# Kernel optimization log

Measured on AMD Instinct MI355X. Metric: run time of the kernel, lower is better.

The kernel has to match this reference:

```python
import jax, jax.numpy as jnp
import numpy as np

B, S, D = 2, 2048, 1024
H, DK = 16, 64


def setup_inputs() -> dict:
    key = jax.random.key(0)
    ks = jax.random.split(key, 10)
    scale = D ** -0.5
    x = jax.random.normal(ks[0], (B, S, D), dtype=jnp.float32)
    mask = jax.random.randint(ks[1], (B, S), 0, 2) > 0  # True = masked positions
    Wq = jax.random.normal(ks[2], (D, H * DK), dtype=jnp.float32) * scale
    Wk = jax.random.normal(ks[3], (D, H * DK), dtype=jnp.float32) * scale
    Wv = jax.random.normal(ks[4], (D, H * DK), dtype=jnp.float32) * scale
    Wo = jax.random.normal(ks[5], (H * DK, D), dtype=jnp.float32) * scale
    bq = jnp.zeros((H * DK,), jnp.float32)
    bk = jnp.zeros((H * DK,), jnp.float32)
    bv = jnp.zeros((H * DK,), jnp.float32)
    bo = jnp.zeros((D,), jnp.float32)
    return {"x": x, "mask": mask, "Wq": Wq, "bq": bq, "Wk": Wk, "bk": bk,
            "Wv": Wv, "bv": bv, "Wo": Wo, "bo": bo}


def reference(x, mask, Wq, bq, Wk, bk, Wv, bv, Wo, bo):
    b, s, _ = x.shape
    # Linear + activation (dropout is identity at eval)
    q = jax.nn.relu(x @ Wq + bq).reshape(b, s, H, DK)
    k = jax.nn.relu(x @ Wk + bk).reshape(b, s, H, DK)
    v = jax.nn.relu(x @ Wv + bv).reshape(b, s, H, DK)
    # scores: [B, H, Sq, Sk]
    attn = jnp.einsum("bqhd,bkhd->bhqk", q, k) * (DK ** -0.5)
    # NOTE: original uses masked_fill(mask, 1e-9) BEFORE softmax (not -inf)
    attn = jnp.where(mask[:, None, None, :], jnp.float32(1e-9), attn)
    attn = jax.nn.softmax(attn, axis=-1)
    out = jnp.einsum("bhqk,bkhd->bqhd", attn, v).reshape(b, s, H * DK)
    return jax.nn.relu(out @ Wo + bo)
```

## Files before the change

kernel.cpp:

```cpp
#include <hip/hip_runtime.h>
#include <stdint.h>

typedef __attribute__((ext_vector_type(8))) short short8;
typedef __attribute__((ext_vector_type(4))) short short4b;
typedef __attribute__((ext_vector_type(4))) float f32x4;

#define MFMA16(a, b, c) __builtin_amdgcn_mfma_f32_16x16x32_bf16((a), (b), (c), 0, 0, 0)

#if defined(__HIP_DEVICE_COMPILE__)
  #if __has_builtin(__builtin_amdgcn_mfma_f32_16x16x16bf16_1k)
    #define MFMA16K16(a, b, c) __builtin_amdgcn_mfma_f32_16x16x16bf16_1k((a), (b), (c), 0, 0, 0)
  #else
    #define MFMA16K16(a, b, c) __builtin_amdgcn_mfma_f32_16x16x16_bf16((a), (b), (c), 0, 0, 0)
  #endif
  #if __has_builtin(__builtin_amdgcn_exp2f)
    #define EXP2(x) __builtin_amdgcn_exp2f(x)
  #else
    #define EXP2(x) exp2f(x)
  #endif
#else
  #define MFMA16K16(a, b, c) (c)
  #define EXP2(x) exp2f(x)
#endif

#define SCL_F (0.125f * 1.44269504f)

__device__ __forceinline__ float b2f(unsigned short u) {
    union { unsigned u; float f; } c; c.u = ((unsigned)u) << 16; return c.f;
}
__device__ __forceinline__ unsigned short f2b(float f) {
    union { float f; unsigned u; } c; c.f = f;
    unsigned r = c.u + 0x7FFF + ((c.u >> 16) & 1);
    return (unsigned short)(r >> 16);
}
__device__ __forceinline__ unsigned f_as_u(float f) {
    union { float f; unsigned u; } c; c.f = f; return c.u;
}

__device__ __forceinline__ void g2lds16(const unsigned short* g, unsigned lds_byte_off) {
    __builtin_amdgcn_global_load_lds(
        (const __attribute__((address_space(1))) void*)(uintptr_t)g,
        (__attribute__((address_space(3))) void*)(uintptr_t)lds_byte_off,
        16, 0, 0);
}

__global__ void detect_dtype(const unsigned short* __restrict__ x, int* __restrict__ flag) {
    __shared__ int cnt;
    if (threadIdx.x == 0) cnt = 0;
    __syncthreads();
    int insane = 0;
    #pragma unroll
    for (int j = 0; j < 4; ++j) {
        unsigned short u = x[threadIdx.x * 4 + j];
        int e = (u >> 7) & 0xFF;
        if ((e >= 1 && e <= 90) || e >= 165) insane++;
    }
    atomicAdd(&cnt, insane);
    __syncthreads();
    if (threadIdx.x == 0) *flag = (cnt > 128) ? 1 : 0;
}

__global__ __launch_bounds__(256) void convtrans_k(const void* __restrict__ s0, const void* __restrict__ s1,
                                                   const void* __restrict__ s2, const void* __restrict__ s3,
                                                   const void* __restrict__ b0, const void* __restrict__ b1,
                                                   const void* __restrict__ b2, const void* __restrict__ b3s,
                                                   const void* __restrict__ xsrc,
                                                   unsigned short* __restrict__ xdst,
                                                   unsigned short* __restrict__ dstBase,
                                                   unsigned short* __restrict__ dstB3,
                                                   unsigned short* __restrict__ dstBo,
                                                   const int* __restrict__ flag) {
    const int z = blockIdx.z;
    if (z >= 5) {
        if (!*flag) return;
        const int slice = z - 5;
        const size_t i0 = (size_t)slice * 524288 + (blockIdx.y * 16 + blockIdx.x) * 2048 + threadIdx.x * 8;
        const float* s = (const float*)xsrc;
        float4 f0 = *(const float4*)&s[i0];
        float4 f1 = *(const float4*)&s[i0 + 4];
        union { short8 v; unsigned short u[8]; } o;
        o.u[0] = f2b(f0.x); o.u[1] = f2b(f0.y); o.u[2] = f2b(f0.z); o.u[3] = f2b(f0.w);
        o.u[4] = f2b(f1.x); o.u[5] = f2b(f1.y); o.u[6] = f2b(f1.z); o.u[7] = f2b(f1.w);
        *(short8*)&xdst[i0] = o.v;
        return;
    }
    if (z == 4) {
        if (blockIdx.y != 0 || blockIdx.x >= 4) return;
        const int w = blockIdx.x;
        const void* src = (w == 0) ? b0 : (w == 1) ? b1 : (w == 2) ? b2 : b3s;
        const float bscl = (w == 0) ? SCL_F : 1.0f;
        #pragma unroll
        for (int j = 0; j < 4; ++j) {
            const int i = threadIdx.x * 4 + j;
            float fv = (*flag) ? ((const float*)src)[i] : b2f(((const unsigned short*)src)[i]);
            unsigned short v = f2b(fv * bscl);
            if (w < 3) dstB3[w * 1024 + i] = v;
            else dstBo[i] = v;
        }
        return;
    }
    __shared__ __align__(16) unsigned short tile[64 * 72];
    const void* src = (z == 0) ? s0 : (z == 1) ? s1 : (z == 2) ? s2 : s3;
    unsigned short* dst = dstBase + (size_t)z * 1024 * 1024;
    const float wscl = (z == 0) ? SCL_F : 1.0f;
    const int tid = threadIdx.x;
    const int r0 = blockIdx.y * 64, c0 = blockIdx.x * 64;
    const int rb = tid >> 3, c = (tid & 7) * 8;
    if (*flag) {
        const float* s = (const float*)src;
        #pragma unroll
        for (int it = 0; it < 2; ++it) {
            int rr = it * 32 + rb;
            float4 f0 = *(const float4*)&s[(size_t)(r0 + rr) * 1024 + c0 + c];
            float4 f1 = *(const float4*)&s[(size_t)(r0 + rr) * 1024 + c0 + c + 4];
            unsigned short* t = &tile[rr * 72 + c];
            t[0] = f2b(f0.x * wscl); t[1] = f2b(f0.y * wscl); t[2] = f2b(f0.z * wscl); t[3] = f2b(f0.w * wscl);
            t[4] = f2b(f1.x * wscl); t[5] = f2b(f1.y * wscl); t[6] = f2b(f1.z * wscl); t[7] = f2b(f1.w * wscl);
        }
    } else if (z == 0) {
        const unsigned short* s = (const unsigned short*)src;
        #pragma unroll
        for (int it = 0; it < 2; ++it) {
            int rr = it * 32 + rb;
            union { short8 v; unsigned short u[8]; } in;
            in.v = *(const short8*)&s[(size_t)(r0 + rr) * 1024 + c0 + c];
            unsigned short* t = &tile[rr * 72 + c];
            #pragma unroll
            for (int j = 0; j < 8; ++j) t[j] = f2b(b2f(in.u[j]) * SCL_F);
        }
    } else {
        const unsigned short* s = (const unsigned short*)src;
        #pragma unroll
        for (int it = 0; it < 2; ++it) {
            int rr = it * 32 + rb;
            *(short8*)&tile[rr * 72 + c] = *(const short8*)&s[(size_t)(r0 + rr) * 1024 + c0 + c];
        }
    }
    __syncthreads();
    #pragma unroll
    for (int it = 0; it < 2; ++it) {
        int n = it * 32 + rb, k8 = c;
        union { short8 s; unsigned short u[8]; } tmp;
        #pragma unroll
        for (int j = 0; j < 8; ++j) tmp.u[j] = tile[(k8 + j) * 72 + n];
        *(short8*)&dst[(size_t)(c0 + n) * 1024 + r0 + k8] = tmp.s;
    }
}

__global__ __launch_bounds__(256) void gemm_qkv(const unsigned short* __restrict__ A,
                                                const void* __restrict__ Araw,
                                                const unsigned short* __restrict__ BT,
                                                const unsigned short* __restrict__ bias,
                                                unsigned short* __restrict__ qkv,
                                                unsigned short* __restrict__ VtG,
                                                const int* __restrict__ mask,
                                                const int* __restrict__ flag,
                                                int K) {
    __shared__ __align__(16) unsigned short smem[24576];
    const int tid = threadIdx.x;
    const int wave = tid >> 6, lane = tid & 63;
    const int quad = lane >> 4, l16 = lane & 15;
    const int wm = wave >> 1, wn = wave & 1;
    const int m0 = blockIdx.y * 128, n0 = blockIdx.x * 128;

    const unsigned short* Ause = (Araw != nullptr && *flag == 0) ? (const unsigned short*)Araw : A;

    f32x4 acc[4][4];
    #pragma unroll
    for (int i = 0; i < 4; i++)
        #pragma unroll
        for (int j = 0; j < 4; j++) acc[i][j] = (f32x4){0.f, 0.f, 0.f, 0.f};

    const int r2 = lane >> 3, sl = lane & 7;
    const int sp = sl ^ r2;
    const int rowl = r2 * 2 + (sp >> 2);
    const int col8 = (sp & 3) * 8;
    const unsigned short* gA0 = Ause + (size_t)(m0 + wave * 32 + rowl) * K + col8;
    const unsigned short* gA1 = gA0 + (size_t)16 * K;
    const unsigned short* gB0 = BT + (size_t)(n0 + wave * 32 + rowl) * K + col8;
    const unsigned short* gB1 = gB0 + (size_t)16 * K;

    const unsigned sA = (unsigned)(uintptr_t)&smem[0];
    const unsigned sB = sA + 24576;
    unsigned lA0 = sA + wave * 2048;
    unsigned lA1 = sA + 8192 + wave * 2048;
    unsigned lA2 = sA + 16384 + wave * 2048;
    unsigned lB0 = sB + wave * 2048;
    unsigned lB1 = sB + 8192 + wave * 2048;
    unsigned lB2 = sB + 16384 + wave * 2048;
    const unsigned short* pA0 = &smem[0];
    const unsigned short* pA1 = &smem[4096];
    const unsigned short* pA2 = &smem[8192];
    const unsigned short* pB0 = &smem[12288];
    const unsigned short* pB1 = &smem[16384];
    const unsigned short* pB2 = &smem[20480];

    const int swz = (((l16 & 1) << 2) | quad) ^ (l16 >> 1);
    const int hp  = l16 >> 1;

    g2lds16(gA0, lA0); g2lds16(gA1, lA0 + 1024);
    g2lds16(gB0, lB0); g2lds16(gB1, lB0 + 1024);
    if (32 < K) {
        g2lds16(gA0 + 32, lA1); g2lds16(gA1 + 32, lA1 + 1024);
        g2lds16(gB0 + 32, lB1); g2lds16(gB1 + 32, lB1 + 1024);
    }
    if (64 < K) {
        g2lds16(gA0 + 64, lA2); g2lds16(gA1 + 64, lA2 + 1024);
        g2lds16(gB0 + 64, lB2); g2lds16(gB1 + 64, lB2 + 1024);
    }

    for (int k0 = 0; k0 < K; k0 += 32) {
        if (k0 + 64 < K)       asm volatile("s_waitcnt vmcnt(8)" ::: "memory");
        else if (k0 + 32 < K)  asm volatile("s_waitcnt vmcnt(4)" ::: "memory");
        else                   asm volatile("s_waitcnt vmcnt(0)" ::: "memory");
        __builtin_amdgcn_s_barrier();

        short8 af[4], bf[4];
        #pragma unroll
        for (int i = 0; i < 4; i++) af[i] = *(const short8*)&pA0[(wm * 32 + i * 8 + hp) * 64 + swz * 8];
        #pragma unroll
        for (int j = 0; j < 4; j++) bf[j] = *(const short8*)&pB0[(wn * 32 + j * 8 + hp) * 64 + swz * 8];
        #pragma unroll
        for (int i = 0; i < 4; i++)
            #pragma unroll
            for (int j = 0; j < 4; j++)
                acc[i][j] = MFMA16(af[i], bf[j], acc[i][j]);

        __builtin_amdgcn_s_barrier();

        if (k0 + 96 < K) {
            g2lds16(gA0 + k0 + 96, lA0); g2lds16(gA1 + k0 + 96, lA0 + 1024);
            g2lds16(gB0 + k0 + 96, lB0); g2lds16(gB1 + k0 + 96, lB0 + 1024);
        }
        unsigned tu;
        tu = lA0; lA0 = lA1; lA1 = lA2; lA2 = tu;
        tu = lB0; lB0 = lB1; lB1 = lB2; lB2 = tu;
        const unsigned short* tp;
        tp = pA0; pA0 = pA1; pA1 = pA2; pA2 = tp;
        tp = pB0; pB0 = pB1; pB1 = pB2; pB2 = tp;
    }

    unsigned short* epi = &smem[0];
    if (n0 >= 2048) {
        #pragma unroll
        for (int j = 0; j < 4; j++) {
            const int cl = wn * 64 + j * 16 + l16;
            const float bj = b2f(bias[n0 + cl]);
            #pragma unroll
            for (int i = 0; i < 4; i++) {
                const int rl = wm * 64 + i * 16 + quad * 4;
                #pragma unroll
                for (int r = 0; r < 4; r++) {
                    float v = acc[i][j][r] + bj;
                    v = v > 0.f ? v : 0.f;
                    epi[cl * 132 + rl + r] = f2b(v);
                }
            }
        }
        __syncthreads();
        const int cl = tid >> 1, half = (tid & 1) * 64;
        const int colg = n0 + cl;
        const int h  = (colg - 2048) >> 6;
        const int dk = (colg - 2048) & 63;
        const int bb = m0 >> 11;
        unsigned short* dst = &VtG[((size_t)(bb * 16 + h) * 64 + dk) * 2048 + (m0 & 2047) + half];
        const unsigned short* src = &epi[cl * 132 + half];
        #pragma unroll
        for (int k = 0; k < 8; k++) *(short8*)&dst[k * 8] = *(const short8*)&src[k * 8];
    } else {
        #pragma unroll
        for (int j = 0; j < 4; j++) {
            const int cl = wn * 64 + j * 16 + l16;
            const float bj = b2f(bias[n0 + cl]);
            #pragma unroll
            for (int i = 0; i < 4; i++) {
                const int rl = wm * 64 + i * 16 + quad * 4;
                #pragma unroll
                for (int r = 0; r < 4; r++) {
                    float v = acc[i][j][r] + bj;
                    v = v > 0.f ? v : 0.f;
                    epi[(rl + r) * 132 + cl] = f2b(v);
                }
            }
        }
        __syncthreads();
        const int row = tid >> 1, half = (tid & 1) * 64;
        const int rowg = m0 + row;
        const int mz = (n0 >= 1024) && mask[rowg];
        unsigned short* dst = &qkv[(size_t)rowg * 3072 + n0 + half];
        const unsigned short* src = &epi[row * 132 + half];
        const short8 zero = {0, 0, 0, 0, 0, 0, 0, 0};
        #pragma unroll
        for (int k = 0; k < 8; k++) *(short8*)&dst[k * 8] = mz ? zero : *(const short8*)&src[k * 8];
    }
}

__global__ __launch_bounds__(256) void gemm64_bias_relu(const unsigned short* __restrict__ A,
                                                        const unsigned short* __restrict__ BT,
                                                        const unsigned short* __restrict__ bias,
                                                        void* __restrict__ C,
                                                        const int* __restrict__ flag,
                                                        int N, int K) {
    __shared__ __align__(16) unsigned short As[3][64 * 32];
    __shared__ __align__(16) unsigned short Bs[3][128 * 32];
    const int tid = threadIdx.x;
    const int wave = tid >> 6, lane = tid & 63;
    const int quad = lane >> 4, l16 = lane & 15;
    const int wm = wave >> 1, wn = wave & 1;
    const int m0 = blockIdx.y * 64, n0 = blockIdx.x * 128;

    f32x4 acc[2][4];
    #pragma unroll
    for (int i = 0; i < 2; i++)
        #pragma unroll
        for (int j = 0; j < 4; j++) acc[i][j] = (f32x4){0.f, 0.f, 0.f, 0.f};

    const int r2 = lane >> 3, sl = lane & 7;
    const int sp = sl ^ r2;
    const int rowl = r2 * 2 + (sp >> 2);
    const int col8 = (sp & 3) * 8;
    const unsigned short* gA0 = A + (size_t)(m0 + wave * 16 + rowl) * K + col8;
    const unsigned short* gB0 = BT + (size_t)(n0 + wave * 32 + rowl) * K + col8;
    const unsigned short* gB1 = gB0 + (size_t)16 * K;

    unsigned lA0 = (unsigned)(uintptr_t)&As[0][0] + wave * 1024;
    unsigned lA1 = (unsigned)(uintptr_t)&As[1][0] + wave * 1024;
    unsigned lA2 = (unsigned)(uintptr_t)&As[2][0] + wave * 1024;
    unsigned lB0 = (unsigned)(uintptr_t)&Bs[0][0] + wave * 2048;
    unsigned lB1 = (unsigned)(uintptr_t)&Bs[1][0] + wave * 2048;
    unsigned lB2 = (unsigned)(uintptr_t)&Bs[2][0] + wave * 2048;
    const unsigned short* pA0 = &As[0][0];
    const unsigned short* pA1 = &As[1][0];
    const unsigned short* pA2 = &As[2][0];
    const unsigned short* pB0 = &Bs[0][0];
    const unsigned short* pB1 = &Bs[1][0];
    const unsigned short* pB2 = &Bs[2][0];

    const int swz = (((l16 & 1) << 2) | quad) ^ (l16 >> 1);
    const int hp  = l16 >> 1;

    g2lds16(gA0, lA0);
    g2lds16(gB0, lB0); g2lds16(gB1, lB0 + 1024);
    if (32 < K) {
        g2lds16(gA0 + 32, lA1);
        g2lds16(gB0 + 32, lB1); g2lds16(gB1 + 32, lB1 + 1024);
    }
    if (64 < K) {
        g2lds16(gA0 + 64, lA2);
        g2lds16(gB0 + 64, lB2); g2lds16(gB1 + 64, lB2 + 1024);
    }

    for (int k0 = 0; k0 < K; k0 += 32) {
        if (k0 + 64 < K)       asm volatile("s_waitcnt vmcnt(6)" ::: "memory");
        else if (k0 + 32 < K)  asm volatile("s_waitcnt vmcnt(3)" ::: "memory");
        else                   asm volatile("s_waitcnt vmcnt(0)" ::: "memory");
        __builtin_amdgcn_s_barrier();

        short8 af[2], bf[4];
        #pragma unroll
        for (int i = 0; i < 2; i++) af[i] = *(const short8*)&pA0[(wm * 16 + i * 8 + hp) * 64 + swz * 8];
        #pragma unroll
        for (int j = 0; j < 4; j++) bf[j] = *(const short8*)&pB0[(wn * 32 + j * 8 + hp) * 64 + swz * 8];
        #pragma unroll
        for (int i = 0; i < 2; i++)
            #pragma unroll
            for (int j = 0; j < 4; j++)
                acc[i][j] = MFMA16(af[i], bf[j], acc[i][j]);

        __builtin_amdgcn_s_barrier();

        if (k0 + 96 < K) {
            g2lds16(gA0 + k0 + 96, lA0);
            g2lds16(gB0 + k0 + 96, lB0); g2lds16(gB1 + k0 + 96, lB0 + 1024);
        }
        unsigned tu;
        tu = lA0; lA0 = lA1; lA1 = lA2; lA2 = tu;
        tu = lB0; lB0 = lB1; lB1 = lB2; lB2 = tu;
        const unsigned short* tp;
        tp = pA0; pA0 = pA1; pA1 = pA2; pA2 = tp;
        tp = pB0; pB0 = pB1; pB1 = pB2; pB2 = tp;
    }

    const int f32out = (*flag != 0);
    #pragma unroll
    for (int j = 0; j < 4; j++) {
        const int col = n0 + wn * 64 + j * 16 + l16;
        const float bj = b2f(bias[col]);
        #pragma unroll
        for (int i = 0; i < 2; i++) {
            const int rowb = m0 + wm * 32 + i * 16 + quad * 4;
            #pragma unroll
            for (int r = 0; r < 4; r++) {
                float v = acc[i][j][r] + bj;
                v = v > 0.f ? v : 0.f;
                if (f32out) ((float*)C)[(size_t)(rowb + r) * N + col] = v;
                else ((unsigned short*)C)[(size_t)(rowb + r) * N + col] = f2b(v);
            }
        }
    }
}

#define ATTN_TILE(Kbuf, Vbuf)                                                            \
    do {                                                                                 \
        __builtin_amdgcn_s_setprio(1);                                                   \
        f32x4 sA[4], sB[4];                                                              \
        _Pragma("unroll")                                                                \
        for (int t = 0; t < 4; ++t) {                                                    \
            const short8 kb0 = *(const short8*)&(Kbuf)[(((t * 16 + l16) * 64) + quad * 8) ^ rx];       \
            const short8 kb1 = *(const short8*)&(Kbuf)[(((t * 16 + l16) * 64) + 32 + quad * 8) ^ rx];  \
            f32x4 z = (f32x4){0.f, 0.f, 0.f, 0.f};                                       \
            sA[t] = MFMA16(kb1, qa1, MFMA16(kb0, qa0, z));                               \
            sB[t] = MFMA16(kb1, qb1, MFMA16(kb0, qb0, z));                               \
        }                                                                                \
        short4b vb[4][4];                                                                \
        _Pragma("unroll")                                                                \
        for (int t = 0; t < 4; ++t)                                                      \
            _Pragma("unroll")                                                            \
            for (int n = 0; n < 4; ++n)                                                  \
                vb[t][n] = *(const short4b*)&(Vbuf)[(((n * 16 + l16) * 64) + t * 16 + quad * 4) ^ rx]; \
        _Pragma("unroll")                                                                \
        for (int t = 0; t < 4; ++t) {                                                    \
            float pA[4], pB[4];                                                          \
            _Pragma("unroll")                                                            \
            for (int r = 0; r < 4; ++r) {                                                \
                pA[r] = EXP2(sA[t][r]);                                                  \
                pB[r] = EXP2(sB[t][r]);                                                  \
            }                                                                            \
            union { unsigned u[2]; short4b s; } fa, fb;                                  \
            fa.u[0] = __builtin_amdgcn_perm(f_as_u(pA[1]), f_as_u(pA[0]), 0x07060302u);  \
            fa.u[1] = __builtin_amdgcn_perm(f_as_u(pA[3]), f_as_u(pA[2]), 0x07060302u);  \
            fb.u[0] = __builtin_amdgcn_perm(f_as_u(pB[1]), f_as_u(pB[0]), 0x07060302u);  \
            fb.u[1] = __builtin_amdgcn_perm(f_as_u(pB[3]), f_as_u(pB[2]), 0x07060302u);  \
            _Pragma("unroll")                                                            \
            for (int n = 0; n < 4; ++n) {                                                \
                oA[n] = MFMA16K16(fa.s, vb[t][n], oA[n]);                                \
                oB[n] = MFMA16K16(fb.s, vb[t][n], oB[n]);                                \
            }                                                                            \
            sumA = MFMA16K16(fa.s, ones, sumA);                                          \
            sumB = MFMA16K16(fb.s, ones, sumB);                                          \
        }                                                                                \
        __builtin_amdgcn_s_setprio(0);                                                   \
    } while (0)

__global__ __launch_bounds__(256) void attn_kernel(const unsigned short* __restrict__ qkv,
                                                   const unsigned short* __restrict__ VtG,
                                                   unsigned short* __restrict__ out) {
    __shared__ __align__(16) unsigned short Ks[2][64 * 64];
    __shared__ __align__(16) unsigned short Vs[2][64 * 64];

    const int l = blockIdx.y * 16 + blockIdx.x;
    const int v = (l & 7) * 64 + (l >> 3);
    const int qt = v & 15, bh = v >> 4;
    const int b = bh >> 4, h = bh & 15;
    const int tid = threadIdx.x, wave = tid >> 6, lane = tid & 63;
    const int quad = lane >> 4, l16 = lane & 15;

    const int qrowA = qt * 128 + wave * 16 + l16;
    const unsigned short* qpA = qkv + (size_t)(b * 2048 + qrowA) * 3072 + h * 64;
    const unsigned short* qpB = qpA + (size_t)64 * 3072;
    const short8 qa0 = *(const short8*)(qpA + quad * 8);
    const short8 qa1 = *(const short8*)(qpA + 32 + quad * 8);
    const short8 qb0 = *(const short8*)(qpB + quad * 8);
    const short8 qb1 = *(const short8*)(qpB + 32 + quad * 8);

    f32x4 oA[4], oB[4], sumA, sumB;
    #pragma unroll
    for (int n = 0; n < 4; n++) { oA[n] = (f32x4){0.f,0.f,0.f,0.f}; oB[n] = (f32x4){0.f,0.f,0.f,0.f}; }
    sumA = (f32x4){0.f,0.f,0.f,0.f};
    sumB = (f32x4){0.f,0.f,0.f,0.f};

    const short4b ones = { (short)0x3F80, (short)0x3F80, (short)0x3F80, (short)0x3F80 };

    const int srow = tid >> 2;
    const int scol = (tid & 3) * 16;
    const int sxor = (srow & 7) << 3;
    const unsigned short* kg = qkv + (size_t)(b * 2048 + srow) * 3072 + 1024 + h * 64 + scol;
    const unsigned short* vg = VtG + (size_t)(bh * 64 + srow) * 2048 + scol;
    const size_t kstep = (size_t)64 * 3072;
    const int sidx0 = (srow * 64 + scol) ^ sxor;
    const int sidx1 = (srow * 64 + scol + 8) ^ sxor;
    unsigned short* wK0a = &Ks[0][sidx0];  unsigned short* wK1a = &Ks[0][sidx1];
    unsigned short* wV0a = &Vs[0][sidx0];  unsigned short* wV1a = &Vs[0][sidx1];
    unsigned short* wK0b = &Ks[1][sidx0];  unsigned short* wK1b = &Ks[1][sidx1];
    unsigned short* wV0b = &Vs[1][sidx0];  unsigned short* wV1b = &Vs[1][sidx1];

    const int rx = (l16 & 7) << 3;

    short8 rkA0 = *(const short8*)(kg);
    short8 rkA1 = *(const short8*)(kg + 8);
    short8 rvA0 = *(const short8*)(vg);
    short8 rvA1 = *(const short8*)(vg + 8);
    *(short8*)wK0a = rkA0;  *(short8*)wK1a = rkA1;
    *(short8*)wV0a = rvA0;  *(short8*)wV1a = rvA1;
    short8 rkB0 = *(const short8*)(kg + kstep);
    short8 rkB1 = *(const short8*)(kg + kstep + 8);
    short8 rvB0 = *(const short8*)(vg + 64);
    short8 rvB1 = *(const short8*)(vg + 64 + 8);
    __syncthreads();

    for (int kt = 0; kt < 32; kt += 2) {
        *(short8*)wK0b = rkB0;  *(short8*)wK1b = rkB1;
        *(short8*)wV0b = rvB0;  *(short8*)wV1b = rvB1;
        if (kt + 2 < 32) {
            rkA0 = *(const short8*)(kg + (kt + 2) * kstep);
            rkA1 = *(const short8*)(kg + (kt + 2) * kstep + 8);
            rvA0 = *(const short8*)(vg + (kt + 2) * 64);
            rvA1 = *(const short8*)(vg + (kt + 2) * 64 + 8);
        }
        ATTN_TILE(Ks[0], Vs[0]);
        __syncthreads();

        if (kt + 2 < 32) {
            *(short8*)wK0a = rkA0;  *(short8*)wK1a = rkA1;
            *(short8*)wV0a = rvA0;  *(short8*)wV1a = rvA1;
        }
        if (kt + 3 < 32) {
            rkB0 = *(const short8*)(kg + (kt + 3) * kstep);
            rkB1 = *(const short8*)(kg + (kt + 3) * kstep + 8);
            rvB0 = *(const short8*)(vg + (kt + 3) * 64);
            rvB1 = *(const short8*)(vg + (kt + 3) * 64 + 8);
        }
        ATTN_TILE(Ks[1], Vs[1]);
        __syncthreads();
    }

    float invA[4], invB[4];
    #pragma unroll
    for (int r = 0; r < 4; ++r) { invA[r] = 1.0f / sumA[r]; invB[r] = 1.0f / sumB[r]; }
    #pragma unroll
    for (int n = 0; n < 4; n++)
        #pragma unroll
        for (int r = 0; r < 4; r++) {
            const int row = qt * 128 + wave * 16 + quad * 4 + r;
            out[(size_t)(b * 2048 + row) * 1024 + h * 64 + n * 16 + l16] = f2b(oA[n][r] * invA[r]);
            out[(size_t)(b * 2048 + row + 64) * 1024 + h * 64 + n * 16 + l16] = f2b(oB[n][r] * invB[r]);
        }
}

extern "C" void kernel_launch(void* const* d_in, const int* in_sizes, int n_in,
                              void* d_out, int out_size, void* d_ws, size_t ws_size,
                              hipStream_t stream) {
    const void* x  = d_in[0];
    const int*  mk = (const int*)d_in[1];
    const void* Wq = d_in[2]; const void* bq = d_in[3];
    const void* Wk = d_in[4]; const void* bk = d_in[5];
    const void* Wv = d_in[6]; const void* bv = d_in[7];
    const void* Wo = d_in[8]; const void* bo = d_in[9];

    char* wsb = (char*)d_ws;
    int* flag = (int*)wsb;
    unsigned short* W0 = (unsigned short*)(wsb + 64);

    const size_t M1 = 1024u * 1024u;
    const size_t M4 = 4096u * 1024u;
    unsigned short* xb  = W0;
    unsigned short* WT  = xb + M4;
    unsigned short* WoT = WT + 3 * M1;
    unsigned short* b3  = WoT + M1;
    unsigned short* bob = b3 + 4096;
    unsigned short* qkv = bob + 1024;
    unsigned short* VtG = qkv + (size_t)4096 * 3072;
    unsigned short* abf = xb;

    detect_dtype<<<1, 256, 0, stream>>>((const unsigned short*)x, flag);

    convtrans_k<<<dim3(16, 16, 13), 256, 0, stream>>>(Wq, Wk, Wv, Wo, bq, bk, bv, bo,
                                                      x, xb, WT, b3, bob, flag);

    gemm_qkv<<<dim3(24, 32), 256, 0, stream>>>(xb, x, WT, b3, qkv, VtG, mk, flag, 1024);
    attn_kernel<<<dim3(16, 32), 256, 0, stream>>>(qkv, VtG, abf);
    gemm64_bias_relu<<<dim3(8, 64), 256, 0, stream>>>(abf, WoT, bob, d_out, flag, 1024, 1024);
}
```

Baseline: 196.2 us.

## Switch output GEMM to double-buffered BK=64 tiles without LDS swizzle

The gemm64_bias_relu kernel moves from a triple-buffered K=32 pipeline to a double-buffered K=64 pipeline, with two MFMA sub-steps per barrier pair. This halves the number of barriers and wait points per K and issues larger batches of global-to-LDS loads. It also drops the XOR swizzle in favour of a plain row-major LDS layout with 128-byte row stride. That layout risks LDS bank conflicts on the short8 fragment reads, and the shallower prefetch depth gives less latency hiding.

```diff
diff --git a/kernel.cpp b/kernel.cpp
--- a/kernel.cpp
+++ b/kernel.cpp
@@ -301,8 +301,8 @@
                                                         void* __restrict__ C,
                                                         const int* __restrict__ flag,
                                                         int N, int K) {
-    __shared__ __align__(16) unsigned short As[3][64 * 32];
-    __shared__ __align__(16) unsigned short Bs[3][128 * 32];
+    __shared__ __align__(16) unsigned short As[2][64 * 64];
+    __shared__ __align__(16) unsigned short Bs[2][128 * 64];
     const int tid = threadIdx.x;
     const int wave = tid >> 6, lane = tid & 63;
     const int quad = lane >> 4, l16 = lane & 15;
@@ -315,70 +315,66 @@
         #pragma unroll
         for (int j = 0; j < 4; j++) acc[i][j] = (f32x4){0.f, 0.f, 0.f, 0.f};
 
-    const int r2 = lane >> 3, sl = lane & 7;
-    const int sp = sl ^ r2;
-    const int rowl = r2 * 2 + (sp >> 2);
-    const int col8 = (sp & 3) * 8;
-    const unsigned short* gA0 = A + (size_t)(m0 + wave * 16 + rowl) * K + col8;
-    const unsigned short* gB0 = BT + (size_t)(n0 + wave * 32 + rowl) * K + col8;
-    const unsigned short* gB1 = gB0 + (size_t)16 * K;
-
-    unsigned lA0 = (unsigned)(uintptr_t)&As[0][0] + wave * 1024;
-    unsigned lA1 = (unsigned)(uintptr_t)&As[1][0] + wave * 1024;
-    unsigned lA2 = (unsigned)(uintptr_t)&As[2][0] + wave * 1024;
-    unsigned lB0 = (unsigned)(uintptr_t)&Bs[0][0] + wave * 2048;
-    unsigned lB1 = (unsigned)(uintptr_t)&Bs[1][0] + wave * 2048;
-    unsigned lB2 = (unsigned)(uintptr_t)&Bs[2][0] + wave * 2048;
-    const unsigned short* pA0 = &As[0][0];
-    const unsigned short* pA1 = &As[1][0];
-    const unsigned short* pA2 = &As[2][0];
-    const unsigned short* pB0 = &Bs[0][0];
-    const unsigned short* pB1 = &Bs[1][0];
-    const unsigned short* pB2 = &Bs[2][0];
-
-    const int swz = (((l16 & 1) << 2) | quad) ^ (l16 >> 1);
-    const int hp  = l16 >> 1;
-
-    g2lds16(gA0, lA0);
-    g2lds16(gB0, lB0); g2lds16(gB1, lB0 + 1024);
-    if (32 < K) {
-        g2lds16(gA0 + 32, lA1);
-        g2lds16(gB0 + 32, lB1); g2lds16(gB1 + 32, lB1 + 1024);
-    }
+    const int lrow = lane >> 3, lch = (lane & 7) * 8;
+    const unsigned short* gA0 = A + (size_t)(m0 + wave * 16 + lrow) * K + lch;
+    const unsigned short* gA1 = gA0 + (size_t)8 * K;
+    const unsigned short* gB0 = BT + (size_t)(n0 + wave * 32 + lrow) * K + lch;
+    const unsigned short* gB1 = gB0 + (size_t)8 * K;
+    const unsigned short* gB2 = gB0 + (size_t)16 * K;
+    const unsigned short* gB3 = gB0 + (size_t)24 * K;
+
+    unsigned aC = (unsigned)(uintptr_t)&As[0][0] + wave * 2048;
+    unsigned aN = (unsigned)(uintptr_t)&As[1][0] + wave * 2048;
+    unsigned bC = (unsigned)(uintptr_t)&Bs[0][0] + wave * 4096;
+    unsigned bN = (unsigned)(uintptr_t)&Bs[1][0] + wave * 4096;
+    const unsigned short* pAc = &As[0][0];
+    const unsigned short* pAn = &As[1][0];
+    const unsigned short* pBc = &Bs[0][0];
+    const unsigned short* pBn = &Bs[1][0];
+
+    g2lds16(gA0, aC); g2lds16(gA1, aC + 1024);
+    g2lds16(gB0, bC); g2lds16(gB1, bC + 1024);
+    g2lds16(gB2, bC + 2048); g2lds16(gB3, bC + 3072);
     if (64 < K) {
-        g2lds16(gA0 + 64, lA2);
-        g2lds16(gB0 + 64, lB2); g2lds16(gB1 + 64, lB2 + 1024);
-    }
-
-    for (int k0 = 0; k0 < K; k0 += 32) {
-        if (k0 + 64 < K)       asm volatile("s_waitcnt vmcnt(6)" ::: "memory");
-        else if (k0 + 32 < K)  asm volatile("s_waitcnt vmcnt(3)" ::: "memory");
-        else                   asm volatile("s_waitcnt vmcnt(0)" ::: "memory");
+        g2lds16(gA0 + 64, aN); g2lds16(gA1 + 64, aN + 1024);
+        g2lds16(gB0 + 64, bN); g2lds16(gB1 + 64, bN + 1024);
+        g2lds16(gB2 + 64, bN + 2048); g2lds16(gB3 + 64, bN + 3072);
+    }
+
+    for (int k0 = 0; k0 < K; k0 += 64) {
+        if (k0 + 64 < K) asm volatile("s_waitcnt vmcnt(6)" ::: "memory");
+        else             asm volatile("s_waitcnt vmcnt(0)" ::: "memory");
         __builtin_amdgcn_s_barrier();
 
-        short8 af[2], bf[4];
-        #pragma unroll
-        for (int i = 0; i < 2; i++) af[i] = *(const short8*)&pA0[(wm * 16 + i * 8 + hp) * 64 + swz * 8];
-        #pragma unroll
-        for (int j = 0; j < 4; j++) bf[j] = *(const short8*)&pB0[(wn * 32 + j * 8 + hp) * 64 + swz * 8];
-        #pragma unroll
-        for (int i = 0; i < 2; i++)
+        #pragma unroll
+        for (int s = 0; s < 2; s++) {
+            short8 af[2], bf[4];
+            #pragma unroll
+            for (int i = 0; i < 2; i++)
+                af[i] = *(const short8*)&pAc[(wm * 32 + i * 16 + l16) * 64 + s * 32 + quad * 8];
             #pragma unroll
             for (int j = 0; j < 4; j++)
-                acc[i][j] = MFMA16(af[i], bf[j], acc[i][j]);
+                bf[j] = *(const short8*)&pBc[(wn * 64 + j * 16 + l16) * 64 + s * 32 + quad * 8];
+            #pragma unroll
+            for (int i = 0; i < 2; i++)
+                #pragma unroll
+                for (int j = 0; j < 4; j++)
+                    acc[i][j] = MFMA16(af[i], bf[j], acc[i][j]);
+        }
 
         __builtin_amdgcn_s_barrier();
 
-        if (k0 + 96 < K) {
-            g2lds16(gA0 + k0 + 96, lA0);
-            g2lds16(gB0 + k0 + 96, lB0); g2lds16(gB1 + k0 + 96, lB0 + 1024);
+        if (k0 + 128 < K) {
+            g2lds16(gA0 + k0 + 128, aC); g2lds16(gA1 + k0 + 128, aC + 1024);
+            g2lds16(gB0 + k0 + 128, bC); g2lds16(gB1 + k0 + 128, bC + 1024);
+            g2lds16(gB2 + k0 + 128, bC + 2048); g2lds16(gB3 + k0 + 128, bC + 3072);
         }
         unsigned tu;
-        tu = lA0; lA0 = lA1; lA1 = lA2; lA2 = tu;
-        tu = lB0; lB0 = lB1; lB1 = lB2; lB2 = tu;
+        tu = aC; aC = aN; aN = tu;
+        tu = bC; bC = bN; bN = tu;
         const unsigned short* tp;
-        tp = pA0; pA0 = pA1; pA1 = pA2; pA2 = tp;
-        tp = pB0; pB0 = pB1; pB1 = pB2; pB2 = tp;
+        tp = pAc; pAc = pAn; pAn = tp;
+        tp = pBc; pBc = pBn; pBn = tp;
     }
 
     const int f32out = (*flag != 0);
```

New measurement: 200.0 us. About the same (+1.9%).

## Fuse fp32-to-bf16 conversion of x into the QKV GEMM A-tile load

Applied to the files above, without the earlier changes.

The separate pass that converts the fp32 input x to bf16 inside the weight conversion kernel is removed. When the input is fp32, the QKV GEMM now streams fp32 A tiles straight into LDS and converts them to bf16 while building the MFMA fragments. This saves a write and a re-read of the bf16 copy of x. In exchange the A tile traffic into LDS doubles, LDS use grows to 72KB, and the conversion work is repeated by each of the 24 column blocks.

```diff
diff --git a/kernel.cpp b/kernel.cpp
--- a/kernel.cpp
+++ b/kernel.cpp
@@ -36,8 +36,14 @@
 __device__ __forceinline__ unsigned f_as_u(float f) {
     union { float f; unsigned u; } c; c.f = f; return c.u;
 }
-
-__device__ __forceinline__ void g2lds16(const unsigned short* g, unsigned lds_byte_off) {
+__device__ __forceinline__ short8 cvt8(float4 a, float4 b) {
+    union { short8 v; unsigned short u[8]; } o;
+    o.u[0] = f2b(a.x); o.u[1] = f2b(a.y); o.u[2] = f2b(a.z); o.u[3] = f2b(a.w);
+    o.u[4] = f2b(b.x); o.u[5] = f2b(b.y); o.u[6] = f2b(b.z); o.u[7] = f2b(b.w);
+    return o.v;
+}
+
+__device__ __forceinline__ void g2lds16(const void* g, unsigned lds_byte_off) {
     __builtin_amdgcn_global_load_lds(
         (const __attribute__((address_space(1))) void*)(uintptr_t)g,
         (__attribute__((address_space(3))) void*)(uintptr_t)lds_byte_off,
@@ -64,26 +70,11 @@
                                                    const void* __restrict__ s2, const void* __restrict__ s3,
                                                    const void* __restrict__ b0, const void* __restrict__ b1,
                                                    const void* __restrict__ b2, const void* __restrict__ b3s,
-                                                   const void* __restrict__ xsrc,
-                                                   unsigned short* __restrict__ xdst,
                                                    unsigned short* __restrict__ dstBase,
                                                    unsigned short* __restrict__ dstB3,
                                                    unsigned short* __restrict__ dstBo,
                                                    const int* __restrict__ flag) {
     const int z = blockIdx.z;
-    if (z >= 5) {
-        if (!*flag) return;
-        const int slice = z - 5;
-        const size_t i0 = (size_t)slice * 524288 + (blockIdx.y * 16 + blockIdx.x) * 2048 + threadIdx.x * 8;
-        const float* s = (const float*)xsrc;
-        float4 f0 = *(const float4*)&s[i0];
-        float4 f1 = *(const float4*)&s[i0 + 4];
-        union { short8 v; unsigned short u[8]; } o;
-        o.u[0] = f2b(f0.x); o.u[1] = f2b(f0.y); o.u[2] = f2b(f0.z); o.u[3] = f2b(f0.w);
-        o.u[4] = f2b(f1.x); o.u[5] = f2b(f1.y); o.u[6] = f2b(f1.z); o.u[7] = f2b(f1.w);
-        *(short8*)&xdst[i0] = o.v;
-        return;
-    }
     if (z == 4) {
         if (blockIdx.y != 0 || blockIdx.x >= 4) return;
         const int w = blockIdx.x;
@@ -147,8 +138,7 @@
     }
 }
 
-__global__ __launch_bounds__(256) void gemm_qkv(const unsigned short* __restrict__ A,
-                                                const void* __restrict__ Araw,
+__global__ __launch_bounds__(256) void gemm_qkv(const void* __restrict__ Araw,
                                                 const unsigned short* __restrict__ BT,
                                                 const unsigned short* __restrict__ bias,
                                                 unsigned short* __restrict__ qkv,
@@ -156,15 +146,13 @@
                                                 const int* __restrict__ mask,
                                                 const int* __restrict__ flag,
                                                 int K) {
-    __shared__ __align__(16) unsigned short smem[24576];
+    __shared__ __align__(16) unsigned short smem[36864];
     const int tid = threadIdx.x;
     const int wave = tid >> 6, lane = tid & 63;
     const int quad = lane >> 4, l16 = lane & 15;
     const int wm = wave >> 1, wn = wave & 1;
     const int m0 = blockIdx.y * 128, n0 = blockIdx.x * 128;
 
-    const unsigned short* Ause = (Araw != nullptr && *flag == 0) ? (const unsigned short*)Araw : A;
-
     f32x4 acc[4][4];
     #pragma unroll
     for (int i = 0; i < 4; i++)
@@ -175,69 +163,141 @@
     const int sp = sl ^ r2;
     const int rowl = r2 * 2 + (sp >> 2);
     const int col8 = (sp & 3) * 8;
-    const unsigned short* gA0 = Ause + (size_t)(m0 + wave * 32 + rowl) * K + col8;
-    const unsigned short* gA1 = gA0 + (size_t)16 * K;
     const unsigned short* gB0 = BT + (size_t)(n0 + wave * 32 + rowl) * K + col8;
     const unsigned short* gB1 = gB0 + (size_t)16 * K;
-
-    const unsigned sA = (unsigned)(uintptr_t)&smem[0];
-    const unsigned sB = sA + 24576;
-    unsigned lA0 = sA + wave * 2048;
-    unsigned lA1 = sA + 8192 + wave * 2048;
-    unsigned lA2 = sA + 16384 + wave * 2048;
-    unsigned lB0 = sB + wave * 2048;
-    unsigned lB1 = sB + 8192 + wave * 2048;
-    unsigned lB2 = sB + 16384 + wave * 2048;
-    const unsigned short* pA0 = &smem[0];
-    const unsigned short* pA1 = &smem[4096];
-    const unsigned short* pA2 = &smem[8192];
-    const unsigned short* pB0 = &smem[12288];
-    const unsigned short* pB1 = &smem[16384];
-    const unsigned short* pB2 = &smem[20480];
-
     const int swz = (((l16 & 1) << 2) | quad) ^ (l16 >> 1);
     const int hp  = l16 >> 1;
 
-    g2lds16(gA0, lA0); g2lds16(gA1, lA0 + 1024);
-    g2lds16(gB0, lB0); g2lds16(gB1, lB0 + 1024);
-    if (32 < K) {
-        g2lds16(gA0 + 32, lA1); g2lds16(gA1 + 32, lA1 + 1024);
-        g2lds16(gB0 + 32, lB1); g2lds16(gB1 + 32, lB1 + 1024);
-    }
-    if (64 < K) {
-        g2lds16(gA0 + 64, lA2); g2lds16(gA1 + 64, lA2 + 1024);
-        g2lds16(gB0 + 64, lB2); g2lds16(gB1 + 64, lB2 + 1024);
-    }
-
-    for (int k0 = 0; k0 < K; k0 += 32) {
-        if (k0 + 64 < K)       asm volatile("s_waitcnt vmcnt(8)" ::: "memory");
-        else if (k0 + 32 < K)  asm volatile("s_waitcnt vmcnt(4)" ::: "memory");
-        else                   asm volatile("s_waitcnt vmcnt(0)" ::: "memory");
-        __builtin_amdgcn_s_barrier();
-
-        short8 af[4], bf[4];
-        #pragma unroll
-        for (int i = 0; i < 4; i++) af[i] = *(const short8*)&pA0[(wm * 32 + i * 8 + hp) * 64 + swz * 8];
-        #pragma unroll
-        for (int j = 0; j < 4; j++) bf[j] = *(const short8*)&pB0[(wn * 32 + j * 8 + hp) * 64 + swz * 8];
-        #pragma unroll
-        for (int i = 0; i < 4; i++)
-            #pragma unroll
-            for (int j = 0; j < 4; j++)
-                acc[i][j] = MFMA16(af[i], bf[j], acc[i][j]);
-
-        __builtin_amdgcn_s_barrier();
-
-        if (k0 + 96 < K) {
-            g2lds16(gA0 + k0 + 96, lA0); g2lds16(gA1 + k0 + 96, lA0 + 1024);
-            g2lds16(gB0 + k0 + 96, lB0); g2lds16(gB1 + k0 + 96, lB0 + 1024);
-        }
-        unsigned tu;
-        tu = lA0; lA0 = lA1; lA1 = lA2; lA2 = tu;
-        tu = lB0; lB0 = lB1; lB1 = lB2; lB2 = tu;
-        const unsigned short* tp;
-        tp = pA0; pA0 = pA1; pA1 = pA2; pA2 = tp;
-        tp = pB0; pB0 = pB1; pB1 = pB2; pB2 = tp;
+    if (*flag) {
+        const float* Af = (const float*)Araw;
+        const int ar  = lane >> 3;
+        const int acg = (lane & 7) ^ ar;
+        const float* gAf = Af + (size_t)(m0 + wave * 32 + ar) * K + acg * 4;
+        const size_t arow8 = (size_t)8 * K;
+
+        const unsigned base = (unsigned)(uintptr_t)&smem[0];
+        unsigned fA0 = base + wave * 4096;
+        unsigned fA1 = fA0 + 16384;
+        unsigned fA2 = fA0 + 32768;
+        unsigned fB0 = base + 49152 + wave * 2048;
+        unsigned fB1 = fB0 + 8192;
+        unsigned fB2 = fB0 + 16384;
+        const char* qA0 = (const char*)&smem[0];
+        const char* qA1 = qA0 + 16384;
+        const char* qA2 = qA0 + 32768;
+        const unsigned short* qB0 = (const unsigned short*)((const char*)&smem[0] + 49152);
+        const unsigned short* qB1 = qB0 + 4096;
+        const unsigned short* qB2 = qB0 + 8192;
+
+        #define STAGE_F32(k0_, lA_, lB_) do {                                   \
+            g2lds16(gAf + (k0_),              (lA_));                           \
+            g2lds16(gAf + (k0_) + arow8,      (lA_) + 1024);                    \
+            g2lds16(gAf + (k0_) + 2 * arow8,  (lA_) + 2048);                    \
+            g2lds16(gAf + (k0_) + 3 * arow8,  (lA_) + 3072);                    \
+            g2lds16(gB0 + (k0_), (lB_));                                        \
+            g2lds16(gB1 + (k0_), (lB_) + 1024);                                 \
+        } while (0)
+
+        STAGE_F32(0, fA0, fB0);
+        if (32 < K) STAGE_F32(32, fA1, fB1);
+        if (64 < K) STAGE_F32(64, fA2, fB2);
+
+        const int h8 = l16 & 7;
+        for (int k0 = 0; k0 < K; k0 += 32) {
+            if (k0 + 64 < K)       asm volatile("s_waitcnt vmcnt(12)" ::: "memory");
+            else if (k0 + 32 < K)  asm volatile("s_waitcnt vmcnt(6)" ::: "memory");
+            else                   asm volatile("s_waitcnt vmcnt(0)" ::: "memory");
+            __builtin_amdgcn_s_barrier();
+
+            short8 af[4], bf[4];
+            #pragma unroll
+            for (int i = 0; i < 4; i++) {
+                const int row = wm * 64 + i * 16 + l16;
+                const float4 a0 = *(const float4*)(qA0 + row * 128 + (((quad * 2 + 0) ^ h8) << 4));
+                const float4 a1 = *(const float4*)(qA0 + row * 128 + (((quad * 2 + 1) ^ h8) << 4));
+                af[i] = cvt8(a0, a1);
+            }
+            #pragma unroll
+            for (int j = 0; j < 4; j++) bf[j] = *(const short8*)&qB0[(wn * 32 + j * 8 + hp) * 64 + swz * 8];
+            #pragma unroll
+            for (int i = 0; i < 4; i++)
+                #pragma unroll
+                for (int j = 0; j < 4; j++)
+                    acc[i][j] = MFMA16(af[i], bf[j], acc[i][j]);
+
+            __builtin_amdgcn_s_barrier();
+
+            if (k0 + 96 < K) STAGE_F32(k0 + 96, fA0, fB0);
+            unsigned tu;
+            tu = fA0; fA0 = fA1; fA1 = fA2; fA2 = tu;
+            tu = fB0; fB0 = fB1; fB1 = fB2; fB2 = tu;
+            const char* tc;
+            tc = qA0; qA0 = qA1; qA1 = qA2; qA2 = tc;
+            const unsigned short* tp;
+            tp = qB0; qB0 = qB1; qB1 = qB2; qB2 = tp;
+        }
+        #undef STAGE_F32
+    } else {
+        const unsigned short* Ab = (const unsigned short*)Araw;
+        const unsigned short* gA0 = Ab + (size_t)(m0 + wave * 32 + rowl) * K + col8;
+        const unsigned short* gA1 = gA0 + (size_t)16 * K;
+
+        const unsigned sA = (unsigned)(uintptr_t)&smem[0];
+        const unsigned sB = sA + 24576;
+        unsigned lA0 = sA + wave * 2048;
+        unsigned lA1 = sA + 8192 + wave * 2048;
+        unsigned lA2 = sA + 16384 + wave * 2048;
+        unsigned lB0 = sB + wave * 2048;
+        unsigned lB1 = sB + 8192 + wave * 2048;
+        unsigned lB2 = sB + 16384 + wave * 2048;
+        const unsigned short* pA0 = &smem[0];
+        const unsigned short* pA1 = &smem[4096];
+        const unsigned short* pA2 = &smem[8192];
+        const unsigned short* pB0 = &smem[12288];
+        const unsigned short* pB1 = &smem[16384];
+        const unsigned short* pB2 = &smem[20480];
+
+        g2lds16(gA0, lA0); g2lds16(gA1, lA0 + 1024);
+        g2lds16(gB0, lB0); g2lds16(gB1, lB0 + 1024);
+        if (32 < K) {
+            g2lds16(gA0 + 32, lA1); g2lds16(gA1 + 32, lA1 + 1024);
+            g2lds16(gB0 + 32, lB1); g2lds16(gB1 + 32, lB1 + 1024);
+        }
+        if (64 < K) {
+            g2lds16(gA0 + 64, lA2); g2lds16(gA1 + 64, lA2 + 1024);
+            g2lds16(gB0 + 64, lB2); g2lds16(gB1 + 64, lB2 + 1024);
+        }
+
+        for (int k0 = 0; k0 < K; k0 += 32) {
+            if (k0 + 64 < K)       asm volatile("s_waitcnt vmcnt(8)" ::: "memory");
+            else if (k0 + 32 < K)  asm volatile("s_waitcnt vmcnt(4)" ::: "memory");
+            else                   asm volatile("s_waitcnt vmcnt(0)" ::: "memory");
+            __builtin_amdgcn_s_barrier();
+
+            short8 af[4], bf[4];
+            #pragma unroll
+            for (int i = 0; i < 4; i++) af[i] = *(const short8*)&pA0[(wm * 32 + i * 8 + hp) * 64 + swz * 8];
+            #pragma unroll
+            for (int j = 0; j < 4; j++) bf[j] = *(const short8*)&pB0[(wn * 32 + j * 8 + hp) * 64 + swz * 8];
+            #pragma unroll
+            for (int i = 0; i < 4; i++)
+                #pragma unroll
+                for (int j = 0; j < 4; j++)
+                    acc[i][j] = MFMA16(af[i], bf[j], acc[i][j]);
+
+            __builtin_amdgcn_s_barrier();
+
+            if (k0 + 96 < K) {
+                g2lds16(gA0 + k0 + 96, lA0); g2lds16(gA1 + k0 + 96, lA0 + 1024);
+                g2lds16(gB0 + k0 + 96, lB0); g2lds16(gB1 + k0 + 96, lB0 + 1024);
+            }
+            unsigned tu;
+            tu = lA0; lA0 = lA1; lA1 = lA2; lA2 = tu;
+            tu = lB0; lB0 = lB1; lB1 = lB2; lB2 = tu;
+            const unsigned short* tp;
+            tp = pA0; pA0 = pA1; pA1 = pA2; pA2 = tp;
+            tp = pB0; pB0 = pB1; pB1 = pB2; pB2 = tp;
+        }
     }
 
     unsigned short* epi = &smem[0];
@@ -564,10 +624,10 @@
 
     detect_dtype<<<1, 256, 0, stream>>>((const unsigned short*)x, flag);
 
-    convtrans_k<<<dim3(16, 16, 13), 256, 0, stream>>>(Wq, Wk, Wv, Wo, bq, bk, bv, bo,
-                                                      x, xb, WT, b3, bob, flag);
-
-    gemm_qkv<<<dim3(24, 32), 256, 0, stream>>>(xb, x, WT, b3, qkv, VtG, mk, flag, 1024);
+    convtrans_k<<<dim3(16, 16, 5), 256, 0, stream>>>(Wq, Wk, Wv, Wo, bq, bk, bv, bo,
+                                                     WT, b3, bob, flag);
+
+    gemm_qkv<<<dim3(24, 32), 256, 0, stream>>>(x, WT, b3, qkv, VtG, mk, flag, 1024);
     attn_kernel<<<dim3(16, 32), 256, 0, stream>>>(qkv, VtG, abf);
     gemm64_bias_relu<<<dim3(8, 64), 256, 0, stream>>>(abf, WoT, bob, d_out, flag, 1024, 1024);
 }
```

Measured after the change: 226.7 us. 1.16x slower.
